# Optimization experiments

Hardware: AMD Instinct MI355X
Metric: run time of the kernel (lower is better)

The kernel has to match this reference:

```python
import jax, jax.numpy as jnp
import numpy as np

B, S, D, H = 2, 2048, 1024, 16
HD = D // H  # head_dim = 64


def setup_inputs() -> dict:
    key = jax.random.key(0)
    ks = jax.random.split(key, 6)
    scale = 1.0 / np.sqrt(D)
    return {
        "x": jax.random.normal(ks[0], (B, S, D), dtype=jnp.float32),
        "Wq": jax.random.normal(ks[1], (D, D), dtype=jnp.float32) * scale,
        "bq": jnp.zeros((D,), dtype=jnp.float32),
        "Wk": jax.random.normal(ks[2], (D, D), dtype=jnp.float32) * scale,
        "bk": jnp.zeros((D,), dtype=jnp.float32),
        "Wv": jax.random.normal(ks[3], (D, D), dtype=jnp.float32) * scale,
        "bv": jnp.zeros((D,), dtype=jnp.float32),
        "Wo": jax.random.normal(ks[4], (D, D), dtype=jnp.float32) * scale,
        "bo": jnp.zeros((D,), dtype=jnp.float32),
    }


def reference(x, Wq, bq, Wk, bk, Wv, bv, Wo, bo):
    b, s, d = x.shape
    # q/k/v projections; torch Linear computes x @ W.T + b (W here stored as [out,in])
    q = (x @ Wq.T + bq).reshape(b, s, H, HD).transpose(0, 2, 1, 3)  # [b,h,s,hd]
    k = (x @ Wk.T + bk).reshape(b, s, H, HD).transpose(0, 2, 1, 3)
    v = (x @ Wv.T + bv).reshape(b, s, H, HD).transpose(0, 2, 1, 3)
    scores = jnp.einsum("bhqd,bhkd->bhqk", q, k) / jnp.sqrt(jnp.float32(HD))
    attn = jax.nn.softmax(scores, axis=-1)  # dropout p=0.0 -> identity
    ctx = jnp.einsum("bhqk,bhkd->bhqd", attn, v)
    ctx = ctx.transpose(0, 2, 1, 3).reshape(b, s, d)
    out = ctx @ Wo.T + bo
    return out, attn
```

## Files before the change

### kernel.cpp

```cpp
#include <hip/hip_runtime.h>
#include <hip/hip_bf16.h>


typedef __attribute__((ext_vector_type(8))) __bf16 bf16x8;
typedef __attribute__((ext_vector_type(8))) short short8;
typedef __attribute__((ext_vector_type(4))) float f32x4;
typedef __attribute__((ext_vector_type(4))) float float4v;
typedef __attribute__((ext_vector_type(4))) unsigned short ushort4v;
typedef __attribute__((ext_vector_type(8))) unsigned short ushort8v;

#define DEV static __device__ __forceinline__

DEV unsigned short f2bf(float f) {
  unsigned int u = __builtin_bit_cast(unsigned int, f);
  u += 0x7FFFu + ((u >> 16) & 1u);
  return (unsigned short)(u >> 16);
}

DEV float exp2v(float x) {
#if __has_builtin(__builtin_amdgcn_exp2f)
  return __builtin_amdgcn_exp2f(x);
#else
  return exp2f(x);
#endif
}

DEV f32x4 mfma16(short8 a, short8 b, f32x4 c) {
  return __builtin_amdgcn_mfma_f32_16x16x32_bf16(
      __builtin_bit_cast(bf16x8, a), __builtin_bit_cast(bf16x8, b), c, 0, 0, 0);
}

DEV void gld16(const void* g, void* l) {
  __builtin_amdgcn_global_load_lds(
      (const __attribute__((address_space(1))) void*)g,
      (__attribute__((address_space(3))) void*)l, 16, 0, 0);
}

#define QSCALE 0.18033688011112042f

__global__ __launch_bounds__(256) void cvt_all(
    const float* __restrict__ x, const float* __restrict__ wq,
    const float* __restrict__ wk, const float* __restrict__ wv,
    const float* __restrict__ wo, unsigned short* __restrict__ xb,
    unsigned short* __restrict__ wqb, unsigned short* __restrict__ wkb,
    unsigned short* __restrict__ wvb, unsigned short* __restrict__ wob) {
  const int bid = blockIdx.x;
  const float* s;
  unsigned short* d;
  int base;
  if (bid < 2048) {
    s = x; d = xb; base = bid * 2048;
  } else {
    const int j = bid - 2048, sel = j >> 9;
    s = sel == 0 ? wq : (sel == 1 ? wk : (sel == 2 ? wv : wo));
    d = sel == 0 ? wqb : (sel == 1 ? wkb : (sel == 2 ? wvb : wob));
    base = (j & 511) * 2048;
  }
  const int i = base + threadIdx.x * 8;
  float4v v0 = *(const float4v*)(s + i);
  float4v v1 = *(const float4v*)(s + i + 4);
  ushort8v o = {f2bf(v0[0]), f2bf(v0[1]), f2bf(v0[2]), f2bf(v0[3]),
                f2bf(v1[0]), f2bf(v1[1]), f2bf(v1[2]), f2bf(v1[3])};
  *(ushort8v*)(d + i) = o;
}

template <int WBF>
__global__ __launch_bounds__(256, 3) void gemm_qkv(
    const unsigned short* __restrict__ xb,
    const void* __restrict__ W0, const void* __restrict__ W1, const void* __restrict__ W2,
    const float* __restrict__ b0, const float* __restrict__ b1, const float* __restrict__ b2,
    unsigned short* __restrict__ Qw, unsigned short* __restrict__ Kw,
    unsigned short* __restrict__ Vt) {
  constexpr int K = 1024;
  __shared__ unsigned short As[2][128 * 32];
  __shared__ unsigned short Bs[2][128 * 32];
  const int tid = threadIdx.x, lane = tid & 63, w = tid >> 6;
  const int g = lane >> 4, ln = lane & 15;
  const int wm = (w >> 1) * 64, wn = (w & 1) * 64;
  const int work = ((int)blockIdx.x & 7) * 96 + ((int)blockIdx.x >> 3);
  const int t = work >> 8, tn = (work >> 5) & 7, tm = work & 31;
  const int m0 = tm * 128, n0 = tn * 128;
  const void* Wsel = t == 0 ? W0 : (t == 1 ? W1 : W2);
  const float* bsel = t == 0 ? b0 : (t == 1 ? b1 : b2);
  const float osc = t == 0 ? QSCALE : 1.0f;

  const unsigned short* Abase = xb + (size_t)(m0 + (tid >> 2)) * K + (tid & 3) * 8;
  const unsigned short* Bb16 = (const unsigned short*)Wsel + (size_t)(n0 + (tid >> 2)) * K + (tid & 3) * 8;
  const float* Bf32 = (const float*)Wsel + (size_t)(n0 + (tid >> 1)) * K + (tid & 1) * 16;
  const int bwoff = (tid >> 1) * 32 + (tid & 1) * 16;

  f32x4 acc[4][4] = {};

  gld16(Abase, &As[0][tid * 8]);
  gld16(Abase + (size_t)64 * K, &As[0][2048 + tid * 8]);
  if (WBF) {
    gld16(Bb16, &Bs[0][tid * 8]);
    gld16(Bb16 + (size_t)64 * K, &Bs[0][2048 + tid * 8]);
  } else {
    float4v u0 = *(const float4v*)Bf32, u1 = *(const float4v*)(Bf32 + 4);
    float4v u2 = *(const float4v*)(Bf32 + 8), u3 = *(const float4v*)(Bf32 + 12);
    ushort8v o0 = {f2bf(u0[0]), f2bf(u0[1]), f2bf(u0[2]), f2bf(u0[3]),
                   f2bf(u1[0]), f2bf(u1[1]), f2bf(u1[2]), f2bf(u1[3])};
    ushort8v o1 = {f2bf(u2[0]), f2bf(u2[1]), f2bf(u2[2]), f2bf(u2[3]),
                   f2bf(u3[0]), f2bf(u3[1]), f2bf(u3[2]), f2bf(u3[3])};
    *(ushort8v*)&Bs[0][bwoff] = o0;
    *(ushort8v*)&Bs[0][bwoff + 8] = o1;
  }

#pragma unroll 2
  for (int it = 0; it < 32; ++it) {
    __syncthreads();
    const int cur = it & 1, nxt = cur ^ 1;
    float4v u0, u1, u2, u3;
    if (it + 1 < 32) {
      const int k1 = (it + 1) * 32;
      gld16(Abase + k1, &As[nxt][tid * 8]);
      gld16(Abase + (size_t)64 * K + k1, &As[nxt][2048 + tid * 8]);
      if (WBF) {
        gld16(Bb16 + k1, &Bs[nxt][tid * 8]);
        gld16(Bb16 + (size_t)64 * K + k1, &Bs[nxt][2048 + tid * 8]);
      } else {
        u0 = *(const float4v*)(Bf32 + k1);
        u1 = *(const float4v*)(Bf32 + k1 + 4);
        u2 = *(const float4v*)(Bf32 + k1 + 8);
        u3 = *(const float4v*)(Bf32 + k1 + 12);
      }
    }
    short8 a[4], bfr[4];
#pragma unroll
    for (int fi = 0; fi < 4; ++fi)
      a[fi] = *(const short8*)&As[cur][(wm + fi * 16 + ln) * 32 + g * 8];
#pragma unroll
    for (int fj = 0; fj < 4; ++fj)
      bfr[fj] = *(const short8*)&Bs[cur][(wn + fj * 16 + ln) * 32 + g * 8];
#pragma unroll
    for (int fi = 0; fi < 4; ++fi)
#pragma unroll
      for (int fj = 0; fj < 4; ++fj) acc[fi][fj] = mfma16(a[fi], bfr[fj], acc[fi][fj]);
    if (!WBF && it + 1 < 32) {
      ushort8v o0 = {f2bf(u0[0]), f2bf(u0[1]), f2bf(u0[2]), f2bf(u0[3]),
                     f2bf(u1[0]), f2bf(u1[1]), f2bf(u1[2]), f2bf(u1[3])};
      ushort8v o1 = {f2bf(u2[0]), f2bf(u2[1]), f2bf(u2[2]), f2bf(u2[3]),
                     f2bf(u3[0]), f2bf(u3[1]), f2bf(u3[2]), f2bf(u3[3])};
      *(ushort8v*)&Bs[nxt][bwoff] = o0;
      *(ushort8v*)&Bs[nxt][bwoff + 8] = o1;
    }
  }

  if (t < 2) {
    unsigned short* Op = t == 0 ? Qw : Kw;
#pragma unroll
    for (int fi = 0; fi < 4; ++fi)
#pragma unroll
      for (int fj = 0; fj < 4; ++fj) {
        const int n = n0 + wn + fj * 16 + ln;
        const float bs = bsel[n];
#pragma unroll
        for (int rr = 0; rr < 4; ++rr) {
          const int m = m0 + wm + fi * 16 + 4 * g + rr;
          Op[(size_t)m * 1024 + n] = f2bf((acc[fi][fj][rr] + bs) * osc);
        }
      }
  } else {
    const int bb = m0 >> 11;
    const int s0 = (m0 & 2047) + wm;
#pragma unroll
    for (int fi = 0; fi < 4; ++fi)
#pragma unroll
      for (int fj = 0; fj < 4; ++fj) {
        const int n = n0 + wn + fj * 16 + ln;
        const float bs = bsel[n];
        ushort4v o = {f2bf(acc[fi][fj][0] + bs), f2bf(acc[fi][fj][1] + bs),
                      f2bf(acc[fi][fj][2] + bs), f2bf(acc[fi][fj][3] + bs)};
        *(ushort4v*)&Vt[(size_t)(bb * 1024 + n) * 2048 + s0 + fi * 16 + 4 * g] = o;
      }
  }
}

template <int WBF>
__global__ __launch_bounds__(256, 3) void gemm_o(const unsigned short* __restrict__ Cw,
                                                 const void* __restrict__ Wo,
                                                 const float* __restrict__ bo,
                                                 float* __restrict__ outp) {
  constexpr int K = 1024;
  __shared__ unsigned short As[2][128 * 32];
  __shared__ unsigned short Bs[2][128 * 32];
  const int tid = threadIdx.x, lane = tid & 63, w = tid >> 6;
  const int g = lane >> 4, ln = lane & 15;
  const int wm = (w >> 1) * 64, wn = (w & 1) * 64;
  const int work = ((int)blockIdx.x & 7) * 32 + ((int)blockIdx.x >> 3);
  const int m0 = (work & 31) * 128, n0 = (work >> 5) * 128;

  const unsigned short* Abase = Cw + (size_t)(m0 + (tid >> 2)) * K + (tid & 3) * 8;
  const unsigned short* Bb16 = (const unsigned short*)Wo + (size_t)(n0 + (tid >> 2)) * K + (tid & 3) * 8;
  const float* Bf32 = (const float*)Wo + (size_t)(n0 + (tid >> 1)) * K + (tid & 1) * 16;
  const int bwoff = (tid >> 1) * 32 + (tid & 1) * 16;

  f32x4 acc[4][4] = {};

  gld16(Abase, &As[0][tid * 8]);
  gld16(Abase + (size_t)64 * K, &As[0][2048 + tid * 8]);
  if (WBF) {
    gld16(Bb16, &Bs[0][tid * 8]);
    gld16(Bb16 + (size_t)64 * K, &Bs[0][2048 + tid * 8]);
  } else {
    float4v u0 = *(const float4v*)Bf32, u1 = *(const float4v*)(Bf32 + 4);
    float4v u2 = *(const float4v*)(Bf32 + 8), u3 = *(const float4v*)(Bf32 + 12);
    ushort8v o0 = {f2bf(u0[0]), f2bf(u0[1]), f2bf(u0[2]), f2bf(u0[3]),
                   f2bf(u1[0]), f2bf(u1[1]), f2bf(u1[2]), f2bf(u1[3])};
    ushort8v o1 = {f2bf(u2[0]), f2bf(u2[1]), f2bf(u2[2]), f2bf(u2[3]),
                   f2bf(u3[0]), f2bf(u3[1]), f2bf(u3[2]), f2bf(u3[3])};
    *(ushort8v*)&Bs[0][bwoff] = o0;
    *(ushort8v*)&Bs[0][bwoff + 8] = o1;
  }

#pragma unroll 2
  for (int it = 0; it < 32; ++it) {
    __syncthreads();
    const int cur = it & 1, nxt = cur ^ 1;
    float4v u0, u1, u2, u3;
    if (it + 1 < 32) {
      const int k1 = (it + 1) * 32;
      gld16(Abase + k1, &As[nxt][tid * 8]);
      gld16(Abase + (size_t)64 * K + k1, &As[nxt][2048 + tid * 8]);
      if (WBF) {
        gld16(Bb16 + k1, &Bs[nxt][tid * 8]);
        gld16(Bb16 + (size_t)64 * K + k1, &Bs[nxt][2048 + tid * 8]);
      } else {
        u0 = *(const float4v*)(Bf32 + k1);
        u1 = *(const float4v*)(Bf32 + k1 + 4);
        u2 = *(const float4v*)(Bf32 + k1 + 8);
        u3 = *(const float4v*)(Bf32 + k1 + 12);
      }
    }
    short8 a[4], bfr[4];
#pragma unroll
    for (int fi = 0; fi < 4; ++fi)
      a[fi] = *(const short8*)&As[cur][(wm + fi * 16 + ln) * 32 + g * 8];
#pragma unroll
    for (int fj = 0; fj < 4; ++fj)
      bfr[fj] = *(const short8*)&Bs[cur][(wn + fj * 16 + ln) * 32 + g * 8];
#pragma unroll
    for (int fi = 0; fi < 4; ++fi)
#pragma unroll
      for (int fj = 0; fj < 4; ++fj) acc[fi][fj] = mfma16(a[fi], bfr[fj], acc[fi][fj]);
    if (!WBF && it + 1 < 32) {
      ushort8v o0 = {f2bf(u0[0]), f2bf(u0[1]), f2bf(u0[2]), f2bf(u0[3]),
                     f2bf(u1[0]), f2bf(u1[1]), f2bf(u1[2]), f2bf(u1[3])};
      ushort8v o1 = {f2bf(u2[0]), f2bf(u2[1]), f2bf(u2[2]), f2bf(u2[3]),
                     f2bf(u3[0]), f2bf(u3[1]), f2bf(u3[2]), f2bf(u3[3])};
      *(ushort8v*)&Bs[nxt][bwoff] = o0;
      *(ushort8v*)&Bs[nxt][bwoff + 8] = o1;
    }
  }

#pragma unroll
  for (int fi = 0; fi < 4; ++fi)
#pragma unroll
    for (int fj = 0; fj < 4; ++fj) {
      const int n = n0 + wn + fj * 16 + ln;
      const float bs = bo[n];
#pragma unroll
      for (int rr = 0; rr < 4; ++rr) {
        const int m = m0 + wm + fi * 16 + 4 * g + rr;
        outp[(size_t)m * 1024 + n] = acc[fi][fj][rr] + bs;
      }
    }
}

__global__ __launch_bounds__(512, 4) void attn_kernel(
    const unsigned short* __restrict__ Qg, const unsigned short* __restrict__ Kg,
    const unsigned short* __restrict__ Vt, float* __restrict__ attn_out,
    unsigned short* __restrict__ ctx) {
  constexpr int LDP = 72;
  __shared__ unsigned short Ps[128 * LDP];
  __shared__ unsigned short Ks[2][64 * 64];
  __shared__ unsigned short Vs[2][64 * 64];
  const int tid = threadIdx.x, lane = tid & 63, w = tid >> 6;
  const int g = lane >> 4, ln = lane & 15;
  const int work = ((int)blockIdx.x & 7) * 64 + ((int)blockIdx.x >> 3);
  const int qt = work & 15, h = (work >> 4) & 15, b = work >> 8;
  const int q0 = qt * 128;
  const size_t kbase = (size_t)b * 2048 * 1024 + (size_t)h * 64;
  const size_t vbase = ((size_t)b * 1024 + h * 64) * 2048;

  for (int cidx = tid; cidx < 1024; cidx += 512) {
    const int r = cidx >> 3, c = (cidx & 7) * 8;
    *(ushort8v*)&Ps[r * LDP + c] =
        *(const ushort8v*)(Qg + kbase + (size_t)(q0 + r) * 1024 + c);
  }
  const int sr = tid >> 3, sb = tid & 7;
  const int swz = ((sb ^ (sr & 7)) * 8);
  const unsigned short* Ksrc = Kg + kbase + (size_t)sr * 1024 + swz;
  const unsigned short* Vsrc = Vt + vbase + (size_t)sr * 2048 + swz;
  __syncthreads();

  short8 qf[2];
#pragma unroll
  for (int hh = 0; hh < 2; ++hh)
    qf[hh] = *(const short8*)&Ps[(w * 16 + ln) * LDP + hh * 32 + 8 * g];

  float lp = 0.f;
  gld16(Ksrc, &Ks[0][tid * 8]);
#pragma unroll 2
  for (int kc = 0; kc < 32; ++kc) {
    __syncthreads();
    if (kc + 1 < 32)
      gld16(Ksrc + (size_t)(kc + 1) * 64 * 1024, &Ks[(kc + 1) & 1][tid * 8]);
    const unsigned short* Kc = Ks[kc & 1];
#pragma unroll
    for (int fk = 0; fk < 4; ++fk) {
      const int row = fk * 16 + ln;
      const short8 kf0 = *(const short8*)&Kc[row * 64 + ((g ^ (ln & 7)) * 8)];
      const short8 kf1 = *(const short8*)&Kc[row * 64 + (((4 + g) ^ (ln & 7)) * 8)];
      f32x4 z = {0.f, 0.f, 0.f, 0.f};
      __builtin_amdgcn_s_setprio(1);
      z = mfma16(kf0, qf[0], z);
      z = mfma16(kf1, qf[1], z);
      __builtin_amdgcn_s_setprio(0);
      lp += exp2v(z[0]) + exp2v(z[1]) + exp2v(z[2]) + exp2v(z[3]);
    }
  }
  lp += __shfl_xor(lp, 16);
  lp += __shfl_xor(lp, 32);
  const float linv = 1.f / lp;

  __syncthreads();
  gld16(Ksrc, &Ks[0][tid * 8]);
  gld16(Vsrc, &Vs[0][tid * 8]);
  f32x4 c_[4] = {};
  const size_t attnbase = ((size_t)(b * 16 + h) * 2048 + q0 + w * 16) * 2048;
#pragma unroll 2
  for (int kc = 0; kc < 32; ++kc) {
    __syncthreads();
    if (kc + 1 < 32) {
      gld16(Ksrc + (size_t)(kc + 1) * 64 * 1024, &Ks[(kc + 1) & 1][tid * 8]);
      gld16(Vsrc + (kc + 1) * 64, &Vs[(kc + 1) & 1][tid * 8]);
    }
    const unsigned short* Kc = Ks[kc & 1];
    const unsigned short* Vc = Vs[kc & 1];
#pragma unroll
    for (int fk = 0; fk < 4; ++fk) {
      const int row = fk * 16 + ln;
      const short8 kf0 = *(const short8*)&Kc[row * 64 + ((g ^ (ln & 7)) * 8)];
      const short8 kf1 = *(const short8*)&Kc[row * 64 + (((4 + g) ^ (ln & 7)) * 8)];
      f32x4 z = {0.f, 0.f, 0.f, 0.f};
      __builtin_amdgcn_s_setprio(1);
      z = mfma16(kf0, qf[0], z);
      z = mfma16(kf1, qf[1], z);
      __builtin_amdgcn_s_setprio(0);
      float4v pv = {exp2v(z[0]) * linv, exp2v(z[1]) * linv, exp2v(z[2]) * linv,
                    exp2v(z[3]) * linv};
      *(float4v*)&attn_out[attnbase + (size_t)ln * 2048 + kc * 64 + fk * 16 + 4 * g] = pv;
      ushort4v pb = {f2bf(pv[0]), f2bf(pv[1]), f2bf(pv[2]), f2bf(pv[3])};
      *(ushort4v*)&Ps[(w * 16 + ln) * LDP + fk * 16 + 4 * g] = pb;
    }
#pragma unroll
    for (int ks = 0; ks < 2; ++ks) {
      const short8 pa = *(const short8*)&Ps[(w * 16 + ln) * LDP + ks * 32 + 8 * g];
      __builtin_amdgcn_s_setprio(1);
#pragma unroll
      for (int fd = 0; fd < 4; ++fd) {
        const int d = fd * 16 + ln;
        const short8 vb = *(const short8*)&Vc[d * 64 + (((ks * 4 + g) ^ (ln & 7)) * 8)];
        c_[fd] = mfma16(pa, vb, c_[fd]);
      }
      __builtin_amdgcn_s_setprio(0);
    }
  }

#pragma unroll
  for (int fd = 0; fd < 4; ++fd)
#pragma unroll
    for (int rr = 0; rr < 4; ++rr) {
      const int q = w * 16 + 4 * g + rr;
      ctx[(size_t)(b * 2048 + q0 + q) * 1024 + h * 64 + fd * 16 + ln] = f2bf(c_[fd][rr]);
    }
}

extern "C" void kernel_launch(void* const* d_in, const int* in_sizes, int n_in,
                              void* d_out, int out_size, void* d_ws, size_t ws_size,
                              hipStream_t stream) {
  const float* x  = (const float*)d_in[0];
  const float* Wq = (const float*)d_in[1];
  const float* bq = (const float*)d_in[2];
  const float* Wk = (const float*)d_in[3];
  const float* bk = (const float*)d_in[4];
  const float* Wv = (const float*)d_in[5];
  const float* bv = (const float*)d_in[6];
  const float* Wo = (const float*)d_in[7];
  const float* bo = (const float*)d_in[8];

  float* outp = (float*)d_out;
  float* attnp = outp + (size_t)4194304;

  unsigned short* Qw = (unsigned short*)d_ws;
  unsigned short* Kw = Qw + (size_t)4194304;
  unsigned short* Vt = Kw + (size_t)4194304;
  unsigned short* Cw = Vt + (size_t)4194304;

  const bool wbf = ws_size >= (size_t)40 * 1024 * 1024;
  dim3 blk(256, 1, 1);

  if (wbf) {
    unsigned short* Wqb = Cw + (size_t)4194304;
    unsigned short* Wkb = Wqb + (size_t)1048576;
    unsigned short* Wvb = Wkb + (size_t)1048576;
    unsigned short* Wob = Wvb + (size_t)1048576;
    cvt_all<<<dim3(4096), blk, 0, stream>>>(x, Wq, Wk, Wv, Wo, Cw, Wqb, Wkb, Wvb, Wob);
    gemm_qkv<1><<<dim3(768), blk, 0, stream>>>(Cw, Wqb, Wkb, Wvb, bq, bk, bv, Qw, Kw, Vt);
    attn_kernel<<<dim3(512), dim3(512), 0, stream>>>(Qw, Kw, Vt, attnp, Cw);
    gemm_o<1><<<dim3(256), blk, 0, stream>>>(Cw, Wob, bo, outp);
  } else {
    cvt_all<<<dim3(2048), blk, 0, stream>>>(x, Wq, Wk, Wv, Wo, Cw, nullptr, nullptr,
                                            nullptr, nullptr);
    gemm_qkv<0><<<dim3(768), blk, 0, stream>>>(Cw, Wq, Wk, Wv, bq, bk, bv, Qw, Kw, Vt);
    attn_kernel<<<dim3(512), dim3(512), 0, stream>>>(Qw, Kw, Vt, attnp, Cw);
    gemm_o<0><<<dim3(256), blk, 0, stream>>>(Cw, Wo, bo, outp);
  }
}
```

Baseline: 245.2 us.

## Halve attention block to 4 waves, each computing 32 query rows

The attention kernel moves from 512 to 256 threads per block, and each wave now handles two 16-row query sub-tiles. Each K/V fragment read from shared memory therefore feeds twice as many MFMAs. Q fragments are loaded straight from global memory into registers, so the shared-memory staging and one barrier go away. The softmax normalisation is folded into the MFMA accumulator init as -log2(l) instead of multiplying every element by 1/l. The trade-off is higher register pressure, fewer waves to hide latency, and each thread issuing twice as many K/V tile loads.

```diff
diff --git a/kernel.cpp b/kernel.cpp
--- a/kernel.cpp
+++ b/kernel.cpp
@@ -268,7 +268,7 @@
     }
 }
 
-__global__ __launch_bounds__(512, 4) void attn_kernel(
+__global__ __launch_bounds__(256, 3) void attn_kernel(
     const unsigned short* __restrict__ Qg, const unsigned short* __restrict__ Kg,
     const unsigned short* __restrict__ Vt, float* __restrict__ attn_out,
     unsigned short* __restrict__ ctx) {
@@ -284,58 +284,71 @@
   const size_t kbase = (size_t)b * 2048 * 1024 + (size_t)h * 64;
   const size_t vbase = ((size_t)b * 1024 + h * 64) * 2048;
 
-  for (int cidx = tid; cidx < 1024; cidx += 512) {
-    const int r = cidx >> 3, c = (cidx & 7) * 8;
-    *(ushort8v*)&Ps[r * LDP + c] =
-        *(const ushort8v*)(Qg + kbase + (size_t)(q0 + r) * 1024 + c);
-  }
+  short8 qf[2][2];
+#pragma unroll
+  for (int s = 0; s < 2; ++s)
+#pragma unroll
+    for (int hh = 0; hh < 2; ++hh)
+      qf[s][hh] = *(const short8*)(Qg + kbase +
+                                   (size_t)(q0 + w * 32 + s * 16 + ln) * 1024 +
+                                   hh * 32 + 8 * g);
+
   const int sr = tid >> 3, sb = tid & 7;
   const int swz = ((sb ^ (sr & 7)) * 8);
   const unsigned short* Ksrc = Kg + kbase + (size_t)sr * 1024 + swz;
   const unsigned short* Vsrc = Vt + vbase + (size_t)sr * 2048 + swz;
-  __syncthreads();
-
-  short8 qf[2];
-#pragma unroll
-  for (int hh = 0; hh < 2; ++hh)
-    qf[hh] = *(const short8*)&Ps[(w * 16 + ln) * LDP + hh * 32 + 8 * g];
-
-  float lp = 0.f;
+
+  float lp0 = 0.f, lp1 = 0.f;
   gld16(Ksrc, &Ks[0][tid * 8]);
+  gld16(Ksrc + (size_t)32 * 1024, &Ks[0][2048 + tid * 8]);
 #pragma unroll 2
   for (int kc = 0; kc < 32; ++kc) {
     __syncthreads();
-    if (kc + 1 < 32)
-      gld16(Ksrc + (size_t)(kc + 1) * 64 * 1024, &Ks[(kc + 1) & 1][tid * 8]);
+    if (kc + 1 < 32) {
+      const unsigned short* s = Ksrc + (size_t)(kc + 1) * 64 * 1024;
+      gld16(s, &Ks[(kc + 1) & 1][tid * 8]);
+      gld16(s + (size_t)32 * 1024, &Ks[(kc + 1) & 1][2048 + tid * 8]);
+    }
     const unsigned short* Kc = Ks[kc & 1];
 #pragma unroll
     for (int fk = 0; fk < 4; ++fk) {
       const int row = fk * 16 + ln;
       const short8 kf0 = *(const short8*)&Kc[row * 64 + ((g ^ (ln & 7)) * 8)];
       const short8 kf1 = *(const short8*)&Kc[row * 64 + (((4 + g) ^ (ln & 7)) * 8)];
-      f32x4 z = {0.f, 0.f, 0.f, 0.f};
+      f32x4 z0 = {0.f, 0.f, 0.f, 0.f}, z1 = {0.f, 0.f, 0.f, 0.f};
       __builtin_amdgcn_s_setprio(1);
-      z = mfma16(kf0, qf[0], z);
-      z = mfma16(kf1, qf[1], z);
+      z0 = mfma16(kf0, qf[0][0], z0);
+      z0 = mfma16(kf1, qf[0][1], z0);
+      z1 = mfma16(kf0, qf[1][0], z1);
+      z1 = mfma16(kf1, qf[1][1], z1);
       __builtin_amdgcn_s_setprio(0);
-      lp += exp2v(z[0]) + exp2v(z[1]) + exp2v(z[2]) + exp2v(z[3]);
-    }
-  }
-  lp += __shfl_xor(lp, 16);
-  lp += __shfl_xor(lp, 32);
-  const float linv = 1.f / lp;
+      lp0 += exp2v(z0[0]) + exp2v(z0[1]) + exp2v(z0[2]) + exp2v(z0[3]);
+      lp1 += exp2v(z1[0]) + exp2v(z1[1]) + exp2v(z1[2]) + exp2v(z1[3]);
+    }
+  }
+  lp0 += __shfl_xor(lp0, 16);
+  lp0 += __shfl_xor(lp0, 32);
+  lp1 += __shfl_xor(lp1, 16);
+  lp1 += __shfl_xor(lp1, 32);
+  const float lb0 = -log2f(lp0), lb1 = -log2f(lp1);
 
   __syncthreads();
   gld16(Ksrc, &Ks[0][tid * 8]);
+  gld16(Ksrc + (size_t)32 * 1024, &Ks[0][2048 + tid * 8]);
   gld16(Vsrc, &Vs[0][tid * 8]);
-  f32x4 c_[4] = {};
-  const size_t attnbase = ((size_t)(b * 16 + h) * 2048 + q0 + w * 16) * 2048;
+  gld16(Vsrc + (size_t)32 * 2048, &Vs[0][2048 + tid * 8]);
+  f32x4 c_[2][4] = {};
+  const size_t attnbase = ((size_t)(b * 16 + h) * 2048 + q0 + w * 32) * 2048;
 #pragma unroll 2
   for (int kc = 0; kc < 32; ++kc) {
     __syncthreads();
     if (kc + 1 < 32) {
-      gld16(Ksrc + (size_t)(kc + 1) * 64 * 1024, &Ks[(kc + 1) & 1][tid * 8]);
-      gld16(Vsrc + (kc + 1) * 64, &Vs[(kc + 1) & 1][tid * 8]);
+      const unsigned short* s = Ksrc + (size_t)(kc + 1) * 64 * 1024;
+      gld16(s, &Ks[(kc + 1) & 1][tid * 8]);
+      gld16(s + (size_t)32 * 1024, &Ks[(kc + 1) & 1][2048 + tid * 8]);
+      const unsigned short* v = Vsrc + (kc + 1) * 64;
+      gld16(v, &Vs[(kc + 1) & 1][tid * 8]);
+      gld16(v + (size_t)32 * 2048, &Vs[(kc + 1) & 1][2048 + tid * 8]);
     }
     const unsigned short* Kc = Ks[kc & 1];
     const unsigned short* Vc = Vs[kc & 1];
@@ -344,38 +357,49 @@
       const int row = fk * 16 + ln;
       const short8 kf0 = *(const short8*)&Kc[row * 64 + ((g ^ (ln & 7)) * 8)];
       const short8 kf1 = *(const short8*)&Kc[row * 64 + (((4 + g) ^ (ln & 7)) * 8)];
-      f32x4 z = {0.f, 0.f, 0.f, 0.f};
+      f32x4 z0 = {lb0, lb0, lb0, lb0}, z1 = {lb1, lb1, lb1, lb1};
       __builtin_amdgcn_s_setprio(1);
-      z = mfma16(kf0, qf[0], z);
-      z = mfma16(kf1, qf[1], z);
+      z0 = mfma16(kf0, qf[0][0], z0);
+      z0 = mfma16(kf1, qf[0][1], z0);
+      z1 = mfma16(kf0, qf[1][0], z1);
+      z1 = mfma16(kf1, qf[1][1], z1);
       __builtin_amdgcn_s_setprio(0);
-      float4v pv = {exp2v(z[0]) * linv, exp2v(z[1]) * linv, exp2v(z[2]) * linv,
-                    exp2v(z[3]) * linv};
-      *(float4v*)&attn_out[attnbase + (size_t)ln * 2048 + kc * 64 + fk * 16 + 4 * g] = pv;
-      ushort4v pb = {f2bf(pv[0]), f2bf(pv[1]), f2bf(pv[2]), f2bf(pv[3])};
-      *(ushort4v*)&Ps[(w * 16 + ln) * LDP + fk * 16 + 4 * g] = pb;
+      float4v pv0 = {exp2v(z0[0]), exp2v(z0[1]), exp2v(z0[2]), exp2v(z0[3])};
+      float4v pv1 = {exp2v(z1[0]), exp2v(z1[1]), exp2v(z1[2]), exp2v(z1[3])};
+      const int coff = kc * 64 + fk * 16 + 4 * g;
+      *(float4v*)&attn_out[attnbase + (size_t)ln * 2048 + coff] = pv0;
+      *(float4v*)&attn_out[attnbase + (size_t)(16 + ln) * 2048 + coff] = pv1;
+      ushort4v pb0 = {f2bf(pv0[0]), f2bf(pv0[1]), f2bf(pv0[2]), f2bf(pv0[3])};
+      ushort4v pb1 = {f2bf(pv1[0]), f2bf(pv1[1]), f2bf(pv1[2]), f2bf(pv1[3])};
+      *(ushort4v*)&Ps[(w * 32 + ln) * LDP + fk * 16 + 4 * g] = pb0;
+      *(ushort4v*)&Ps[(w * 32 + 16 + ln) * LDP + fk * 16 + 4 * g] = pb1;
     }
 #pragma unroll
     for (int ks = 0; ks < 2; ++ks) {
-      const short8 pa = *(const short8*)&Ps[(w * 16 + ln) * LDP + ks * 32 + 8 * g];
+      const short8 pa0 = *(const short8*)&Ps[(w * 32 + ln) * LDP + ks * 32 + 8 * g];
+      const short8 pa1 = *(const short8*)&Ps[(w * 32 + 16 + ln) * LDP + ks * 32 + 8 * g];
       __builtin_amdgcn_s_setprio(1);
 #pragma unroll
       for (int fd = 0; fd < 4; ++fd) {
         const int d = fd * 16 + ln;
         const short8 vb = *(const short8*)&Vc[d * 64 + (((ks * 4 + g) ^ (ln & 7)) * 8)];
-        c_[fd] = mfma16(pa, vb, c_[fd]);
+        c_[0][fd] = mfma16(pa0, vb, c_[0][fd]);
+        c_[1][fd] = mfma16(pa1, vb, c_[1][fd]);
       }
       __builtin_amdgcn_s_setprio(0);
     }
   }
 
 #pragma unroll
-  for (int fd = 0; fd < 4; ++fd)
-#pragma unroll
-    for (int rr = 0; rr < 4; ++rr) {
-      const int q = w * 16 + 4 * g + rr;
-      ctx[(size_t)(b * 2048 + q0 + q) * 1024 + h * 64 + fd * 16 + ln] = f2bf(c_[fd][rr]);
-    }
+  for (int s = 0; s < 2; ++s)
+#pragma unroll
+    for (int fd = 0; fd < 4; ++fd)
+#pragma unroll
+      for (int rr = 0; rr < 4; ++rr) {
+        const int q = w * 32 + s * 16 + 4 * g + rr;
+        ctx[(size_t)(b * 2048 + q0 + q) * 1024 + h * 64 + fd * 16 + ln] =
+            f2bf(c_[s][fd][rr]);
+      }
 }
 
 extern "C" void kernel_launch(void* const* d_in, const int* in_sizes, int n_in,
@@ -409,13 +433,13 @@
     unsigned short* Wob = Wvb + (size_t)1048576;
     cvt_all<<<dim3(4096), blk, 0, stream>>>(x, Wq, Wk, Wv, Wo, Cw, Wqb, Wkb, Wvb, Wob);
     gemm_qkv<1><<<dim3(768), blk, 0, stream>>>(Cw, Wqb, Wkb, Wvb, bq, bk, bv, Qw, Kw, Vt);
-    attn_kernel<<<dim3(512), dim3(512), 0, stream>>>(Qw, Kw, Vt, attnp, Cw);
+    attn_kernel<<<dim3(512), blk, 0, stream>>>(Qw, Kw, Vt, attnp, Cw);
     gemm_o<1><<<dim3(256), blk, 0, stream>>>(Cw, Wob, bo, outp);
   } else {
     cvt_all<<<dim3(2048), blk, 0, stream>>>(x, Wq, Wk, Wv, Wo, Cw, nullptr, nullptr,
                                             nullptr, nullptr);
     gemm_qkv<0><<<dim3(768), blk, 0, stream>>>(Cw, Wq, Wk, Wv, bq, bk, bv, Qw, Kw, Vt);
-    attn_kernel<<<dim3(512), dim3(512), 0, stream>>>(Qw, Kw, Vt, attnp, Cw);
+    attn_kernel<<<dim3(512), blk, 0, stream>>>(Qw, Kw, Vt, attnp, Cw);
     gemm_o<0><<<dim3(256), blk, 0, stream>>>(Cw, Wo, bo, outp);
   }
 }
```

Measured after the change: 256.3 us. 1.05x slower.
